# Kernel tuning notes

Measured on AMD Instinct MI355X. Metric: run time of the kernel, lower is better.

## Reference

```python
import jax, jax.numpy as jnp
import numpy as np

N_A, N_B = 100000, 50000
F_IN, C = 32, 64
L, G = 2, 4  # conv layers per gate, gates (i,f,o,c)
E_AA, E_AB, E_BB = 1600000, 800000, 800000


def setup_inputs() -> dict:
    key = jax.random.key(0)
    ks = jax.random.split(key, 15)
    return {
        "x_a": jax.random.normal(ks[0], (N_A, F_IN), jnp.float32),
        "x_b": jax.random.normal(ks[1], (N_B, F_IN), jnp.float32),
        "c_a": jax.random.normal(ks[2], (N_A, C), jnp.float32),
        "c_b": jax.random.normal(ks[3], (N_B, C), jnp.float32),
        "lin_w": jax.random.normal(ks[4], (G, 2, F_IN, C), jnp.float32) * 0.1,
        "lin_b": jax.random.uniform(ks[5], (G, 2, C), jnp.float32),
        "conv_wl": jax.random.normal(ks[6], (G, L, 3, C, C), jnp.float32) * 0.1,
        "conv_wr": jax.random.normal(ks[7], (G, L, 3, C, C), jnp.float32) * 0.1,
        "conv_b": jax.random.uniform(ks[8], (G, L, 3, C), jnp.float32) * 0.1,
        "src_aa": jax.random.randint(ks[9], (E_AA,), 0, N_A),
        "dst_aa": jax.random.randint(ks[10], (E_AA,), 0, N_A),
        "src_ab": jax.random.randint(ks[11], (E_AB,), 0, N_A),
        "dst_ab": jax.random.randint(ks[12], (E_AB,), 0, N_B),
        "src_bb": jax.random.randint(ks[13], (E_BB,), 0, N_B),
        "dst_bb": jax.random.randint(ks[14], (E_BB,), 0, N_B),
    }


def _seg_mean(x_src, src, dst, n_dst):
    # SAGEConv mean aggregation; empty destinations get 0 (PyG semantics)
    s = jax.ops.segment_sum(x_src[src], dst, num_segments=n_dst)
    cnt = jax.ops.segment_sum(jnp.ones((src.shape[0], 1), x_src.dtype), dst, num_segments=n_dst)
    return s / jnp.maximum(cnt, 1.0)


def _gate(g, x_a, x_b, lin_w, lin_b, conv_wl, conv_wr, conv_b, idx):
    src_aa, dst_aa, src_ab, dst_ab, src_bb, dst_bb = idx
    t_a = x_a @ lin_w[g, 0]
    t_b = x_b @ lin_w[g, 1]
    for l in range(L):
        # edge type 0: a->a (dst a)
        agg_aa = _seg_mean(t_a, src_aa, dst_aa, N_A)
        na = agg_aa @ conv_wl[g, l, 0] + t_a @ conv_wr[g, l, 0] + conv_b[g, l, 0]
        # edge types 1: a->b and 2: b->b, HeteroConv sums both into dst b
        agg_ab = _seg_mean(t_a, src_ab, dst_ab, N_B)
        agg_bb = _seg_mean(t_b, src_bb, dst_bb, N_B)
        nb = (agg_ab @ conv_wl[g, l, 1] + t_b @ conv_wr[g, l, 1] + conv_b[g, l, 1]
              + agg_bb @ conv_wl[g, l, 2] + t_b @ conv_wr[g, l, 2] + conv_b[g, l, 2])
        t_a, t_b = na, nb
    return lin_b[g, 0] + t_a, lin_b[g, 1] + t_b


def reference(x_a, x_b, c_a, c_b, lin_w, lin_b, conv_wl, conv_wr, conv_b,
              src_aa, dst_aa, src_ab, dst_ab, src_bb, dst_bb):
    idx = (src_aa, dst_aa, src_ab, dst_ab, src_bb, dst_bb)
    i_a, i_b = map(jax.nn.sigmoid, _gate(0, x_a, x_b, lin_w, lin_b, conv_wl, conv_wr, conv_b, idx))
    f_a, f_b = map(jax.nn.sigmoid, _gate(1, x_a, x_b, lin_w, lin_b, conv_wl, conv_wr, conv_b, idx))
    o_a, o_b = map(jax.nn.sigmoid, _gate(2, x_a, x_b, lin_w, lin_b, conv_wl, conv_wr, conv_b, idx))
    g_a, g_b = map(jnp.tanh, _gate(3, x_a, x_b, lin_w, lin_b, conv_wl, conv_wr, conv_b, idx))
    cn_a = f_a * c_a + i_a * g_a
    cn_b = f_b * c_b + i_b * g_b
    h_a = o_a * jnp.tanh(cn_a)
    h_b = o_b * jnp.tanh(cn_b)
    return (h_a, h_b, cn_a, cn_b)
```

## Files before the change

### kernel.cpp

```cpp
#include <hip/hip_runtime.h>
#include <hip/hip_bf16.h>

#define NA 100000
#define NB 50000
#define EAA 1600000
#define EAB 800000
#define EBB 800000

#define NBKAA 782
#define NBKB  391
#define EPB 2000
#define BKA 800
#define BKB 400
#define DCAP 4096

#define GF2A 782
#define GF2B 391

typedef __hip_bfloat16 bf16;
typedef __attribute__((ext_vector_type(8))) short bf16x8;
typedef __attribute__((ext_vector_type(4))) float f32x4;

__device__ __forceinline__ float u2f(unsigned short u) {
  union { unsigned int i; float f; } x; x.i = ((unsigned int)u) << 16; return x.f;
}
__device__ __forceinline__ unsigned short f2u(float f) {
  __hip_bfloat16 h = __float2bfloat16(f);
  return *reinterpret_cast<unsigned short*>(&h);
}
__device__ __forceinline__ short f2bs(float f) {
  __hip_bfloat16 h = __float2bfloat16(f);
  return *reinterpret_cast<short*>(&h);
}
__device__ __forceinline__ float fast_sigmoid(float z) {
  return 1.f / (1.f + __expf(-z));
}
__device__ __forceinline__ float fast_tanh(float z) {
  z = fminf(fmaxf(z, -15.f), 15.f);
  float t = __expf(2.f * z);
  return (t - 1.f) / (t + 1.f);
}

__global__ __launch_bounds__(256) void kA_bin(
    const int* __restrict__ d1, const int* __restrict__ d2, const int* __restrict__ d3,
    int* __restrict__ binAA, int* __restrict__ binAB, int* __restrict__ binBB) {
  __shared__ int h[1024];
  int blk = blockIdx.x;
  const int* dst; int* out; int e0, nbk;
  if (blk < BKA)            { dst = d1; out = binAA + blk * NBKAA; e0 = blk * EPB; nbk = NBKAA; }
  else if (blk < BKA + BKB) { int k = blk - BKA; dst = d2; out = binAB + k * NBKB; e0 = k * EPB; nbk = NBKB; }
  else                      { int k = blk - BKA - BKB; dst = d3; out = binBB + k * NBKB; e0 = k * EPB; nbk = NBKB; }
  for (int i = threadIdx.x; i < nbk; i += 256) h[i] = 0;
  __syncthreads();
  for (int i = threadIdx.x; i < EPB; i += 256) atomicAdd(&h[dst[e0 + i] >> 7], 1);
  __syncthreads();
  for (int i = threadIdx.x; i < nbk; i += 256) out[i] = h[i];
}

__global__ __launch_bounds__(256) void kB1(
    int* __restrict__ binAA, int* __restrict__ binAB, int* __restrict__ binBB,
    int* __restrict__ totAA, int* __restrict__ totAB, int* __restrict__ totBB) {
  int wave = threadIdx.x >> 6, lane = threadIdx.x & 63;
  int wid = blockIdx.x * 4 + wave;
  int* bin; int* tot; int b, nblk, nbk;
  if (wid < NBKAA)              { bin = binAA; tot = totAA; b = wid; nblk = BKA; nbk = NBKAA; }
  else if (wid < NBKAA + NBKB)  { bin = binAB; tot = totAB; b = wid - NBKAA; nblk = BKB; nbk = NBKB; }
  else                          { bin = binBB; tot = totBB; b = wid - NBKAA - NBKB; nblk = BKB; nbk = NBKB; }
  int C = (nblk + 63) / 64;
  int vals[16]; int s = 0;
  for (int j = 0; j < C; ++j) { int k = lane * C + j; vals[j] = (k < nblk) ? bin[k * nbk + b] : 0; s += vals[j]; }
  int pre = s;
  for (int o = 1; o < 64; o <<= 1) { int x = __shfl_up(pre, o); if (lane >= o) pre += x; }
  int run = pre - s;
  for (int j = 0; j < C; ++j) { int k = lane * C + j; if (k < nblk) { int v = vals[j]; bin[k * nbk + b] = run; run += v; } }
  if (lane == 63) tot[b] = pre;
}

__global__ __launch_bounds__(256) void kB2(
    const int* __restrict__ totAA, const int* __restrict__ totAB, const int* __restrict__ totBB,
    int* __restrict__ bsAA, int* __restrict__ bsAB, int* __restrict__ bsBB) {
  __shared__ int part[256];
  int set = blockIdx.x; const int* tot; int* bs; int nbk;
  if (set == 0)      { tot = totAA; bs = bsAA; nbk = NBKAA; }
  else if (set == 1) { tot = totAB; bs = bsAB; nbk = NBKB; }
  else               { tot = totBB; bs = bsBB; nbk = NBKB; }
  int t = threadIdx.x;
  int v[4]; int s = 0;
  #pragma unroll
  for (int j = 0; j < 4; ++j) { int k = t * 4 + j; v[j] = (k < nbk) ? tot[k] : 0; s += v[j]; }
  part[t] = s;
  __syncthreads();
  for (int o = 1; o < 256; o <<= 1) {
    int x = (t >= o) ? part[t - o] : 0;
    __syncthreads();
    part[t] += x;
    __syncthreads();
  }
  int run = part[t] - s;
  #pragma unroll
  for (int j = 0; j < 4; ++j) { int k = t * 4 + j; if (k < nbk) { bs[k] = run; run += v[j]; } }
  if (t == 255) bs[nbk] = part[255];
}

__global__ __launch_bounds__(256) void kC_scatter(
    const int* __restrict__ s1, const int* __restrict__ d1,
    const int* __restrict__ s2, const int* __restrict__ d2,
    const int* __restrict__ s3, const int* __restrict__ d3,
    const int* __restrict__ binAA, const int* __restrict__ binAB, const int* __restrict__ binBB,
    const int* __restrict__ bsAA, const int* __restrict__ bsAB, const int* __restrict__ bsBB,
    int* __restrict__ pkAA, int* __restrict__ pkAB, int* __restrict__ pkBB) {
  __shared__ int baseL[1024];
  __shared__ int run[1024];
  int blk = blockIdx.x;
  const int* src; const int* dst; const int* bin; const int* bs; int* pk; int e0, nbk, bofs;
  if (blk < BKA)            { src = s1; dst = d1; bin = binAA; bs = bsAA; pk = pkAA; e0 = blk * EPB; nbk = NBKAA; bofs = blk * NBKAA; }
  else if (blk < BKA + BKB) { int k = blk - BKA; src = s2; dst = d2; bin = binAB; bs = bsAB; pk = pkAB; e0 = k * EPB; nbk = NBKB; bofs = k * NBKB; }
  else                      { int k = blk - BKA - BKB; src = s3; dst = d3; bin = binBB; bs = bsBB; pk = pkBB; e0 = k * EPB; nbk = NBKB; bofs = k * NBKB; }
  for (int i = threadIdx.x; i < nbk; i += 256) { baseL[i] = bs[i] + bin[bofs + i]; run[i] = 0; }
  __syncthreads();
  for (int i = threadIdx.x; i < EPB; i += 256) {
    int d = dst[e0 + i];
    int b = d >> 7;
    int off = atomicAdd(&run[b], 1);
    pk[baseL[b] + off] = src[e0 + i] | ((d & 127) << 24);
  }
}

__global__ __launch_bounds__(256) void kD_nodesort(
    const int* __restrict__ pkAA, const int* __restrict__ pkAB, const int* __restrict__ pkBB,
    const int* __restrict__ bsAA, const int* __restrict__ bsAB, const int* __restrict__ bsBB,
    int* __restrict__ colAA, int* __restrict__ colAB, int* __restrict__ colBB,
    int* __restrict__ stAA, int* __restrict__ ctAA,
    int* __restrict__ stAB, int* __restrict__ ctAB,
    int* __restrict__ stBB, int* __restrict__ ctBB) {
  __shared__ int hist[128], nodeOff[129], run[128];
  __shared__ int stage[DCAP];
  int wid = blockIdx.x;
  const int* pk; const int* bs; int* col; int* stn; int* ctn; int b, N;
  if (wid < NBKAA)             { pk = pkAA; bs = bsAA; col = colAA; stn = stAA; ctn = ctAA; b = wid; N = NA; }
  else if (wid < NBKAA + NBKB) { pk = pkAB; bs = bsAB; col = colAB; stn = stAB; ctn = ctAB; b = wid - NBKAA; N = NB; }
  else                         { pk = pkBB; bs = bsBB; col = colBB; stn = stBB; ctn = ctBB; b = wid - NBKAA - NBKB; N = NB; }
  int node0 = b * 128;
  int base = bs[b], cntB = bs[b + 1] - base;
  int t = threadIdx.x;
  if (t < 128) hist[t] = 0;
  __syncthreads();
  for (int i = t; i < cntB; i += 256) atomicAdd(&hist[pk[base + i] >> 24], 1);
  __syncthreads();
  if (t < 64) {
    int v0 = hist[2 * t], v1 = hist[2 * t + 1];
    int s = v0 + v1; int pre = s;
    for (int o = 1; o < 64; o <<= 1) { int x = __shfl_up(pre, o); if (t >= o) pre += x; }
    int ex = pre - s;
    nodeOff[2 * t] = ex; nodeOff[2 * t + 1] = ex + v0;
    if (t == 63) nodeOff[128] = pre;
    run[2 * t] = 0; run[2 * t + 1] = 0;
  }
  __syncthreads();
  if (t < 128) {
    int n = node0 + t;
    if (n < N) { ctn[n] = hist[t]; stn[n] = base + nodeOff[t]; }
  }
  if (cntB <= DCAP) {
    for (int i = t; i < cntB; i += 256) {
      int e = pk[base + i]; int ln = e >> 24;
      int off = atomicAdd(&run[ln], 1);
      stage[nodeOff[ln] + off] = e & 0xFFFFFF;
    }
    __syncthreads();
    for (int i = t; i < cntB; i += 256) col[base + i] = stage[i];
  } else {
    for (int i = t; i < cntB; i += 256) {
      int e = pk[base + i]; int ln = e >> 24;
      int off = atomicAdd(&run[ln], 1);
      col[base + nodeOff[ln] + off] = e & 0xFFFFFF;
    }
  }
}

__global__ __launch_bounds__(256) void k_cast2(const float* __restrict__ xa, const float* __restrict__ xb,
                                               bf16* __restrict__ ya, bf16* __restrict__ yb) {
  int i = blockIdx.x * 256 + threadIdx.x;
  const float* x; bf16* y; int base;
  if (i < 800000)       { x = xa; y = ya; base = i * 4; }
  else if (i < 1200000) { x = xb; y = yb; base = (i - 800000) * 4; }
  else return;
  float4 v = *(const float4*)(x + base);
  ushort4 o; o.x = f2u(v.x); o.y = f2u(v.y); o.z = f2u(v.z); o.w = f2u(v.w);
  *(ushort4*)(y + base) = o;
}

__global__ __launch_bounds__(256) void kW1(
    const float* __restrict__ lin_w, const float* __restrict__ wl, const float* __restrict__ wr,
    float* __restrict__ Mbuf) {
  __shared__ float Ls[32][64];
  __shared__ float Rs[64][64];
  int id = blockIdx.x, term = id >> 2, g = id & 3;
  const float* L = lin_w + ((size_t)g * 2 + (term >= 3 ? 1 : 0)) * 2048;
  const float* R1; const float* R2 = nullptr;
  switch (term) {
    case 0: R1 = wl + ((size_t)(g * 2) * 3 + 0) * 4096; break;
    case 1: R1 = wr + ((size_t)(g * 2) * 3 + 0) * 4096; break;
    case 2: R1 = wl + ((size_t)(g * 2) * 3 + 1) * 4096; break;
    case 3: R1 = wl + ((size_t)(g * 2) * 3 + 2) * 4096; break;
    default: R1 = wr + ((size_t)(g * 2) * 3 + 1) * 4096; R2 = wr + ((size_t)(g * 2) * 3 + 2) * 4096; break;
  }
  for (int i = threadIdx.x; i < 2048; i += 256) Ls[i >> 6][i & 63] = L[i];
  for (int i = threadIdx.x; i < 4096; i += 256) Rs[i >> 6][i & 63] = R2 ? (R1[i] + R2[i]) : R1[i];
  __syncthreads();
  int c = threadIdx.x & 63, rq = threadIdx.x >> 6;
  float acc[8] = {0, 0, 0, 0, 0, 0, 0, 0};
  for (int k = 0; k < 64; ++k) {
    float rv = Rs[k][c];
    #pragma unroll
    for (int i = 0; i < 8; ++i) acc[i] += Ls[rq * 8 + i][k] * rv;
  }
  #pragma unroll
  for (int i = 0; i < 8; ++i)
    Mbuf[(size_t)(term * 4 + g) * 2048 + (rq * 8 + i) * 64 + c] = acc[i];
}

__global__ __launch_bounds__(256) void kW2(
    const float* __restrict__ Mbuf, const float* __restrict__ wl, const float* __restrict__ wr,
    const float* __restrict__ cbv, const float* __restrict__ lin_b,
    bf16* __restrict__ Wfrag, float* __restrict__ Bv) {
  __shared__ float Ps[2][32][65];
  __shared__ float Ws[2][64][64];
  int blk = blockIdx.x;
  if (blk >= 36) {
    int g = blk - 36;
    if (threadIdx.x < 64) {
      int c = threadIdx.x;
      const float* b00 = cbv + (size_t)((g * 2 + 0) * 3 + 0) * 64;
      const float* b10 = cbv + (size_t)((g * 2 + 0) * 3 + 1) * 64;
      const float* b20 = cbv + (size_t)((g * 2 + 0) * 3 + 2) * 64;
      const float* b01 = cbv + (size_t)((g * 2 + 1) * 3 + 0) * 64;
      const float* b11 = cbv + (size_t)((g * 2 + 1) * 3 + 1) * 64;
      const float* b21 = cbv + (size_t)((g * 2 + 1) * 3 + 2) * 64;
      const float* wl01 = wl + (size_t)((g * 2 + 1) * 3 + 0) * 4096;
      const float* wl11 = wl + (size_t)((g * 2 + 1) * 3 + 1) * 4096;
      const float* wl21 = wl + (size_t)((g * 2 + 1) * 3 + 2) * 4096;
      const float* wr01 = wr + (size_t)((g * 2 + 1) * 3 + 0) * 4096;
      const float* wr11 = wr + (size_t)((g * 2 + 1) * 3 + 1) * 4096;
      const float* wr21 = wr + (size_t)((g * 2 + 1) * 3 + 2) * 4096;
      float s_maa = 0.f, s_ca = 0.f, s_mab = 0.f, s_mbb = 0.f, s_cb = 0.f;
      for (int k = 0; k < 64; ++k) {
        float v0 = b00[k], vb = b10[k] + b20[k];
        s_maa += v0 * wl01[k * 64 + c];
        s_ca  += v0 * wr01[k * 64 + c];
        s_mab += v0 * wl11[k * 64 + c];
        s_mbb += vb * wl21[k * 64 + c];
        s_cb  += vb * (wr11[k * 64 + c] + wr21[k * 64 + c]);
      }
      Bv[(g * 5 + 0) * 64 + c] = s_maa;
      Bv[(g * 5 + 1) * 64 + c] = s_ca + b01[c] + lin_b[(g * 2 + 0) * 64 + c];
      Bv[(g * 5 + 2) * 64 + c] = s_mab;
      Bv[(g * 5 + 3) * 64 + c] = s_mbb;
      Bv[(g * 5 + 4) * 64 + c] = s_cb + b11[c] + b21[c] + lin_b[(g * 2 + 1) * 64 + c];
    }
    return;
  }
  int mat = blk, g, m;
  if (blk < 12) { g = blk / 3; m = blk % 3; }
  else          { g = (blk - 12) / 6; m = (blk - 12) % 6 + 3; }
  const float* wl01 = wl + (size_t)((g * 2 + 1) * 3 + 0) * 4096;
  const float* wl11 = wl + (size_t)((g * 2 + 1) * 3 + 1) * 4096;
  const float* wl21 = wl + (size_t)((g * 2 + 1) * 3 + 2) * 4096;
  const float* wr01 = wr + (size_t)((g * 2 + 1) * 3 + 0) * 4096;
  const float* wr11 = wr + (size_t)((g * 2 + 1) * 3 + 1) * 4096;
  const float* wr21 = wr + (size_t)((g * 2 + 1) * 3 + 2) * 4096;
  int   p1t, p2t = -1;
  const float *w1a = nullptr, *w1b = nullptr, *w2a = nullptr, *w2b = nullptr;
  switch (m) {
    case 0: p1t = 0; w1a = wl01; break;
    case 1: p1t = 1; w1a = wl01; p2t = 0; w2a = wr01; break;
    case 2: p1t = 1; w1a = wr01; break;
    case 3: p1t = 0; w1a = wl11; break;
    case 4: p1t = 1; w1a = wl11; p2t = 2; w2a = wr11; w2b = wr21; break;
    case 5: p1t = 2; w1a = wl21; break;
    case 6: p1t = 3; w1a = wl21; break;
    case 7: p1t = 3; w1a = wr11; w1b = wr21; p2t = 4; w2a = wl21; break;
    default: p1t = 4; w1a = wr11; w1b = wr21; break;
  }
  int nprod = (p2t >= 0) ? 2 : 1;
  for (int i = threadIdx.x; i < 2048; i += 256) Ps[0][i >> 6][i & 63] = Mbuf[(size_t)(p1t * 4 + g) * 2048 + i];
  for (int i = threadIdx.x; i < 4096; i += 256) Ws[0][i >> 6][i & 63] = w1b ? (w1a[i] + w1b[i]) : w1a[i];
  if (nprod == 2) {
    for (int i = threadIdx.x; i < 2048; i += 256) Ps[1][i >> 6][i & 63] = Mbuf[(size_t)(p2t * 4 + g) * 2048 + i];
    for (int i = threadIdx.x; i < 4096; i += 256) Ws[1][i >> 6][i & 63] = w2b ? (w2a[i] + w2b[i]) : w2a[i];
  }
  __syncthreads();
  int nt = threadIdx.x >> 6, lane = threadIdx.x & 63;
  int c = nt * 16 + (lane & 15), kb = (lane >> 4) * 8;
  float acc[8] = {0, 0, 0, 0, 0, 0, 0, 0};
  for (int k = 0; k < 64; ++k) {
    float w1v = Ws[0][k][c];
    #pragma unroll
    for (int j = 0; j < 8; ++j) acc[j] += Ps[0][kb + j][k] * w1v;
  }
  if (nprod == 2) {
    for (int k = 0; k < 64; ++k) {
      float w2v = Ws[1][k][c];
      #pragma unroll
      for (int j = 0; j < 8; ++j) acc[j] += Ps[1][kb + j][k] * w2v;
    }
  }
  bf16x8 v;
  #pragma unroll
  for (int j = 0; j < 8; ++j) v[j] = f2bs(acc[j]);
  *(bf16x8*)(Wfrag + ((size_t)(mat * 4 + nt) * 64 + lane) * 8) = v;
}

__device__ __forceinline__ void acc8(float* s, uint4 v) {
  s[0] += u2f((unsigned short)(v.x & 0xFFFF)); s[1] += u2f((unsigned short)(v.x >> 16));
  s[2] += u2f((unsigned short)(v.y & 0xFFFF)); s[3] += u2f((unsigned short)(v.y >> 16));
  s[4] += u2f((unsigned short)(v.z & 0xFFFF)); s[5] += u2f((unsigned short)(v.z >> 16));
  s[6] += u2f((unsigned short)(v.w & 0xFFFF)); s[7] += u2f((unsigned short)(v.w >> 16));
}
__device__ __forceinline__ void red16(float* s) {
  #pragma unroll
  for (int j = 0; j < 8; ++j) {
    s[j] += __shfl_xor(s[j], 4);
    s[j] += __shfl_xor(s[j], 8);
    s[j] += __shfl_xor(s[j], 16);
    s[j] += __shfl_xor(s[j], 32);
  }
}
__device__ __forceinline__ uint4 pack8(const float* s, float inv) {
  uint4 o;
  o.x = (unsigned)f2u(s[0] * inv) | ((unsigned)f2u(s[1] * inv) << 16);
  o.y = (unsigned)f2u(s[2] * inv) | ((unsigned)f2u(s[3] * inv) << 16);
  o.z = (unsigned)f2u(s[4] * inv) | ((unsigned)f2u(s[5] * inv) << 16);
  o.w = (unsigned)f2u(s[6] * inv) | ((unsigned)f2u(s[7] * inv) << 16);
  return o;
}

__global__ __launch_bounds__(256) void k_aggP1(
    const bf16* __restrict__ xa, const bf16* __restrict__ xb,
    bf16* __restrict__ P, bf16* __restrict__ Q, bf16* __restrict__ R,
    const int* __restrict__ st_aa, const int* __restrict__ ct_aa, const int* __restrict__ col_aa,
    const int* __restrict__ st_ab, const int* __restrict__ ct_ab, const int* __restrict__ col_ab,
    const int* __restrict__ st_bb, const int* __restrict__ ct_bb, const int* __restrict__ col_bb) {
  int b = blockIdx.x;
  const bf16* src; bf16* dst; const int* start; const int* cnt; const int* col; int n0;
  if (b < 25000)      { src = xa; dst = P; start = st_aa; cnt = ct_aa; col = col_aa; n0 = b * 4; }
  else if (b < 37500) { src = xa; dst = Q; start = st_ab; cnt = ct_ab; col = col_ab; n0 = (b - 25000) * 4; }
  else                { src = xb; dst = R; start = st_bb; cnt = ct_bb; col = col_bb; n0 = (b - 37500) * 4; }
  int wave = threadIdx.x >> 6, lane = threadIdx.x & 63;
  int n = n0 + wave;
  int e16 = lane >> 2, c4 = lane & 3;
  int st = start[n];
  int deg = cnt[n];
  float s[8] = {0, 0, 0, 0, 0, 0, 0, 0};
  for (int e = e16; e < deg; e += 16) {
    int i = col[st + e];
    uint4 v = *(const uint4*)(src + (size_t)i * 32 + c4 * 8);
    acc8(s, v);
  }
  red16(s);
  if (e16 == 0) {
    float inv = 1.f / (float)(deg > 1 ? deg : 1);
    *(uint4*)(dst + (size_t)n * 32 + c4 * 8) = pack8(s, inv);
  }
}

__global__ __launch_bounds__(256) void k_aggP2(
    const bf16* __restrict__ P, const bf16* __restrict__ Q, const bf16* __restrict__ R,
    bf16* __restrict__ P2, bf16* __restrict__ Q2, bf16* __restrict__ S, bf16* __restrict__ T,
    const int* __restrict__ st_aa, const int* __restrict__ ct_aa, const int* __restrict__ col_aa,
    const int* __restrict__ st_ab, const int* __restrict__ ct_ab, const int* __restrict__ col_ab,
    const int* __restrict__ st_bb, const int* __restrict__ ct_bb, const int* __restrict__ col_bb) {
  int b = blockIdx.x;
  int wave = threadIdx.x >> 6, lane = threadIdx.x & 63;
  int e16 = lane >> 2, c4 = lane & 3;
  if (b < 37500) {
    const bf16* src; bf16* dst; const int* start; const int* cnt; const int* col; int n0;
    if (b < 25000) { src = P; dst = P2; start = st_aa; cnt = ct_aa; col = col_aa; n0 = b * 4; }
    else           { src = P; dst = Q2; start = st_ab; cnt = ct_ab; col = col_ab; n0 = (b - 25000) * 4; }
    int n = n0 + wave;
    int st = start[n];
    int deg = cnt[n];
    float s[8] = {0, 0, 0, 0, 0, 0, 0, 0};
    for (int e = e16; e < deg; e += 16) {
      int i = col[st + e];
      uint4 v = *(const uint4*)(src + (size_t)i * 32 + c4 * 8);
      acc8(s, v);
    }
    red16(s);
    if (e16 == 0) {
      float inv = 1.f / (float)(deg > 1 ? deg : 1);
      *(uint4*)(dst + (size_t)n * 32 + c4 * 8) = pack8(s, inv);
    }
  } else {
    int n = (b - 37500) * 4 + wave;
    int st = st_bb[n];
    int deg = ct_bb[n];
    float sq[8] = {0, 0, 0, 0, 0, 0, 0, 0};
    float sr[8] = {0, 0, 0, 0, 0, 0, 0, 0};
    for (int e = e16; e < deg; e += 16) {
      int i = col_bb[st + e];
      uint4 vq = *(const uint4*)(Q + (size_t)i * 32 + c4 * 8);
      uint4 vr = *(const uint4*)(R + (size_t)i * 32 + c4 * 8);
      acc8(sq, vq);
      acc8(sr, vr);
    }
    red16(sq);
    red16(sr);
    if (e16 == 0) {
      float inv = 1.f / (float)(deg > 1 ? deg : 1);
      *(uint4*)(S + (size_t)n * 32 + c4 * 8) = pack8(sq, inv);
      *(uint4*)(T + (size_t)n * 32 + c4 * 8) = pack8(sr, inv);
    }
  }
}

__global__ __launch_bounds__(256) void k_fin(
    const bf16* __restrict__ xa, const bf16* __restrict__ P, const bf16* __restrict__ P2,
    const bf16* __restrict__ xb, const bf16* __restrict__ Q, const bf16* __restrict__ R,
    const bf16* __restrict__ Q2, const bf16* __restrict__ S, const bf16* __restrict__ T,
    const bf16* __restrict__ Wfrag, const float* __restrict__ Bv,
    const int* __restrict__ cnt_aa, const int* __restrict__ cnt_ab, const int* __restrict__ cnt_bb,
    const float* __restrict__ c_a, const float* __restrict__ c_b,
    float* __restrict__ out) {
  int blk = blockIdx.x;
  int wave = threadIdx.x >> 6, lane = threadIdx.x & 63;
  int l15 = lane & 15, l4 = lane >> 4;
  const size_t TOTA = (size_t)NA * 64, TOTB = (size_t)NB * 64;
  #define FRAG(mat, nt) (*(const bf16x8*)(Wfrag + ((size_t)((mat) * 4 + (nt)) * 64 + lane) * 8))
  const bf16x8 z8 = {0, 0, 0, 0, 0, 0, 0, 0};

  if (blk < GF2A) {
    int row0 = (blk * 4 + wave) * 32;
    bf16x8 a[3][2];
    float m[2][4];
    #pragma unroll
    for (int s = 0; s < 2; ++s) {
      int r = row0 + s * 16 + l15;
      bool ok = r < NA;
      a[0][s] = ok ? *(const bf16x8*)(P2 + (size_t)r * 32 + l4 * 8) : z8;
      a[1][s] = ok ? *(const bf16x8*)(P  + (size_t)r * 32 + l4 * 8) : z8;
      a[2][s] = ok ? *(const bf16x8*)(xa + (size_t)r * 32 + l4 * 8) : z8;
      #pragma unroll
      for (int q = 0; q < 4; ++q) {
        int rr = row0 + s * 16 + l4 * 4 + q;
        m[s][q] = (rr < NA && cnt_aa[rr] > 0) ? 1.f : 0.f;
      }
    }
    float* h = out;
    float* cn = out + TOTA + TOTB;
    #pragma unroll
    for (int nt = 0; nt < 4; ++nt) {
      int col = nt * 16 + l15;
      bf16x8 fr[12];
      #pragma unroll
      for (int gq = 0; gq < 12; ++gq) fr[gq] = FRAG(gq, nt);
      float bm[4], bc[4];
      #pragma unroll
      for (int g = 0; g < 4; ++g) { bm[g] = Bv[(g * 5 + 0) * 64 + col]; bc[g] = Bv[(g * 5 + 1) * 64 + col]; }
      #pragma unroll
      for (int s = 0; s < 2; ++s) {
        float cpre[4];
        #pragma unroll
        for (int q = 0; q < 4; ++q) {
          int rr = row0 + s * 16 + l4 * 4 + q;
          cpre[q] = (rr < NA) ? c_a[(size_t)rr * 64 + col] : 0.f;
        }
        f32x4 z[4];
        #pragma unroll
        for (int g = 0; g < 4; ++g) {
          f32x4 acc = {0.f, 0.f, 0.f, 0.f};
          acc = __builtin_amdgcn_mfma_f32_16x16x32_bf16(a[0][s], fr[g * 3 + 0], acc, 0, 0, 0);
          acc = __builtin_amdgcn_mfma_f32_16x16x32_bf16(a[1][s], fr[g * 3 + 1], acc, 0, 0, 0);
          acc = __builtin_amdgcn_mfma_f32_16x16x32_bf16(a[2][s], fr[g * 3 + 2], acc, 0, 0, 0);
          z[g] = acc;
        }
        #pragma unroll
        for (int q = 0; q < 4; ++q) {
          int rr = row0 + s * 16 + l4 * 4 + q;
          if (rr >= NA) continue;
          float zi = z[0][q] + m[s][q] * bm[0] + bc[0];
          float zf = z[1][q] + m[s][q] * bm[1] + bc[1];
          float zo = z[2][q] + m[s][q] * bm[2] + bc[2];
          float zg = z[3][q] + m[s][q] * bm[3] + bc[3];
          float ig = fast_sigmoid(zi);
          float fg = fast_sigmoid(zf);
          float og = fast_sigmoid(zo);
          float gg = fast_tanh(zg);
          size_t idx = (size_t)rr * 64 + col;
          float cv = fg * cpre[q] + ig * gg;
          h[idx] = og * fast_tanh(cv);
          cn[idx] = cv;
        }
      }
    }
  } else {
    int bb = blk - GF2A;
    int row0 = (bb * 4 + wave) * 32;
    bf16x8 a[6][2];
    float mab[2][4], mbb[2][4];
    #pragma unroll
    for (int s = 0; s < 2; ++s) {
      int r = row0 + s * 16 + l15;
      bool ok = r < NB;
      a[0][s] = ok ? *(const bf16x8*)(Q2 + (size_t)r * 32 + l4 * 8) : z8;
      a[1][s] = ok ? *(const bf16x8*)(Q  + (size_t)r * 32 + l4 * 8) : z8;
      a[2][s] = ok ? *(const bf16x8*)(S  + (size_t)r * 32 + l4 * 8) : z8;
      a[3][s] = ok ? *(const bf16x8*)(T  + (size_t)r * 32 + l4 * 8) : z8;
      a[4][s] = ok ? *(const bf16x8*)(R  + (size_t)r * 32 + l4 * 8) : z8;
      a[5][s] = ok ? *(const bf16x8*)(xb + (size_t)r * 32 + l4 * 8) : z8;
      #pragma unroll
      for (int q = 0; q < 4; ++q) {
        int rr = row0 + s * 16 + l4 * 4 + q;
        bool okr = rr < NB;
        mab[s][q] = (okr && cnt_ab[rr] > 0) ? 1.f : 0.f;
        mbb[s][q] = (okr && cnt_bb[rr] > 0) ? 1.f : 0.f;
      }
    }
    float* h = out + TOTA;
    float* cn = out + 2 * TOTA + TOTB;
    #pragma unroll
    for (int nt = 0; nt < 4; ++nt) {
      int col = nt * 16 + l15;
      float bm1[4], bm2[4], bc[4];
      #pragma unroll
      for (int g = 0; g < 4; ++g) {
        bm1[g] = Bv[(g * 5 + 2) * 64 + col];
        bm2[g] = Bv[(g * 5 + 3) * 64 + col];
        bc[g]  = Bv[(g * 5 + 4) * 64 + col];
      }
      float cpre[2][4];
      #pragma unroll
      for (int s = 0; s < 2; ++s)
        #pragma unroll
        for (int q = 0; q < 4; ++q) {
          int rr = row0 + s * 16 + l4 * 4 + q;
          cpre[s][q] = (rr < NB) ? c_b[(size_t)rr * 64 + col] : 0.f;
        }
      f32x4 z[2][4];
      #pragma unroll
      for (int s = 0; s < 2; ++s)
        #pragma unroll
        for (int g = 0; g < 4; ++g) z[s][g] = (f32x4){0.f, 0.f, 0.f, 0.f};
      #pragma unroll
      for (int g = 0; g < 4; ++g) {
        bf16x8 fr[6];
        #pragma unroll
        for (int t = 0; t < 6; ++t) fr[t] = FRAG(12 + g * 6 + t, nt);
        #pragma unroll
        for (int s = 0; s < 2; ++s) {
          #pragma unroll
          for (int t = 0; t < 6; ++t)
            z[s][g] = __builtin_amdgcn_mfma_f32_16x16x32_bf16(a[t][s], fr[t], z[s][g], 0, 0, 0);
        }
      }
      #pragma unroll
      for (int s = 0; s < 2; ++s) {
        #pragma unroll
        for (int q = 0; q < 4; ++q) {
          int rr = row0 + s * 16 + l4 * 4 + q;
          if (rr >= NB) continue;
          float zi = z[s][0][q] + mab[s][q] * bm1[0] + mbb[s][q] * bm2[0] + bc[0];
          float zf = z[s][1][q] + mab[s][q] * bm1[1] + mbb[s][q] * bm2[1] + bc[1];
          float zo = z[s][2][q] + mab[s][q] * bm1[2] + mbb[s][q] * bm2[2] + bc[2];
          float zg = z[s][3][q] + mab[s][q] * bm1[3] + mbb[s][q] * bm2[3] + bc[3];
          float ig = fast_sigmoid(zi);
          float fg = fast_sigmoid(zf);
          float og = fast_sigmoid(zo);
          float gg = fast_tanh(zg);
          size_t idx = (size_t)rr * 64 + col;
          float cv = fg * cpre[s][q] + ig * gg;
          h[idx] = og * fast_tanh(cv);
          cn[idx] = cv;
        }
      }
    }
  }
  #undef FRAG
}

extern "C" void kernel_launch(void* const* d_in, const int* in_sizes, int n_in,
                              void* d_out, int out_size, void* d_ws, size_t ws_size,
                              hipStream_t stream) {
  (void)in_sizes; (void)n_in; (void)out_size; (void)ws_size;
  const float* x_a    = (const float*)d_in[0];
  const float* x_b    = (const float*)d_in[1];
  const float* c_a    = (const float*)d_in[2];
  const float* c_b    = (const float*)d_in[3];
  const float* lin_w  = (const float*)d_in[4];
  const float* lin_b  = (const float*)d_in[5];
  const float* conv_wl = (const float*)d_in[6];
  const float* conv_wr = (const float*)d_in[7];
  const float* conv_cb = (const float*)d_in[8];
  const int* src_aa = (const int*)d_in[9];
  const int* dst_aa = (const int*)d_in[10];
  const int* src_ab = (const int*)d_in[11];
  const int* dst_ab = (const int*)d_in[12];
  const int* src_bb = (const int*)d_in[13];
  const int* dst_bb = (const int*)d_in[14];

  char* ws = (char*)d_ws;
  size_t off = 0;
  auto alloc = [&](size_t bytes) -> char* {
    off = (off + 255) & ~(size_t)255;
    char* p = ws + off;
    off += bytes;
    return p;
  };
  bf16* xab = (bf16*)alloc((size_t)NA * 32 * 2);
  bf16* xbb = (bf16*)alloc((size_t)NB * 32 * 2);
  bf16* P   = (bf16*)alloc((size_t)NA * 32 * 2);
  bf16* P2  = (bf16*)alloc((size_t)NA * 32 * 2);
  bf16* Q   = (bf16*)alloc((size_t)NB * 32 * 2);
  bf16* R   = (bf16*)alloc((size_t)NB * 32 * 2);
  bf16* Q2  = (bf16*)alloc((size_t)NB * 32 * 2);
  bf16* S   = (bf16*)alloc((size_t)NB * 32 * 2);
  bf16* T   = (bf16*)alloc((size_t)NB * 32 * 2);
  float* Mbuf = (float*)alloc((size_t)20 * 2048 * 4);
  bf16* Wfrag = (bf16*)alloc((size_t)36 * 4 * 64 * 8 * 2);
  float* Bv = (float*)alloc((size_t)4 * 5 * 64 * 4);
  int* col_aa  = (int*)alloc((size_t)EAA * 4);
  int* col_ab  = (int*)alloc((size_t)EAB * 4);
  int* col_bb  = (int*)alloc((size_t)EBB * 4);
  int* pk_aa   = (int*)alloc((size_t)EAA * 4);
  int* pk_ab   = (int*)alloc((size_t)EAB * 4);
  int* pk_bb   = (int*)alloc((size_t)EBB * 4);
  int* start_aa = (int*)alloc((size_t)NA * 4);
  int* start_ab = (int*)alloc((size_t)NB * 4);
  int* start_bb = (int*)alloc((size_t)NB * 4);
  int* cnt_aa  = (int*)alloc((size_t)NA * 4);
  int* cnt_ab  = (int*)alloc((size_t)NB * 4);
  int* cnt_bb  = (int*)alloc((size_t)NB * 4);
  int* binAA   = (int*)alloc((size_t)BKA * NBKAA * 4);
  int* binAB   = (int*)alloc((size_t)BKB * NBKB * 4);
  int* binBB   = (int*)alloc((size_t)BKB * NBKB * 4);
  int* totAA   = (int*)alloc((size_t)NBKAA * 4);
  int* totAB   = (int*)alloc((size_t)NBKB * 4);
  int* totBB   = (int*)alloc((size_t)NBKB * 4);
  int* bsAA    = (int*)alloc((size_t)(NBKAA + 1) * 4);
  int* bsAB    = (int*)alloc((size_t)(NBKB + 1) * 4);
  int* bsBB    = (int*)alloc((size_t)(NBKB + 1) * 4);

  kW1<<<20, 256, 0, stream>>>(lin_w, conv_wl, conv_wr, Mbuf);
  kW2<<<40, 256, 0, stream>>>(Mbuf, conv_wl, conv_wr, conv_cb, lin_b, Wfrag, Bv);
  k_cast2<<<4688, 256, 0, stream>>>(x_a, x_b, xab, xbb);

  kA_bin<<<BKA + 2 * BKB, 256, 0, stream>>>(dst_aa, dst_ab, dst_bb, binAA, binAB, binBB);
  kB1<<<(NBKAA + 2 * NBKB) / 4, 256, 0, stream>>>(binAA, binAB, binBB, totAA, totAB, totBB);
  kB2<<<3, 256, 0, stream>>>(totAA, totAB, totBB, bsAA, bsAB, bsBB);
  kC_scatter<<<BKA + 2 * BKB, 256, 0, stream>>>(src_aa, dst_aa, src_ab, dst_ab, src_bb, dst_bb,
                                                binAA, binAB, binBB, bsAA, bsAB, bsBB,
                                                pk_aa, pk_ab, pk_bb);
  kD_nodesort<<<NBKAA + 2 * NBKB, 256, 0, stream>>>(pk_aa, pk_ab, pk_bb, bsAA, bsAB, bsBB,
                                                    col_aa, col_ab, col_bb,
                                                    start_aa, cnt_aa, start_ab, cnt_ab,
                                                    start_bb, cnt_bb);

  k_aggP1<<<50000, 256, 0, stream>>>(xab, xbb, P, Q, R,
                                     start_aa, cnt_aa, col_aa,
                                     start_ab, cnt_ab, col_ab,
                                     start_bb, cnt_bb, col_bb);
  k_aggP2<<<50000, 256, 0, stream>>>(P, Q, R, P2, Q2, S, T,
                                     start_aa, cnt_aa, col_aa,
                                     start_ab, cnt_ab, col_ab,
                                     start_bb, cnt_bb, col_bb);

  k_fin<<<GF2A + GF2B, 256, 0, stream>>>(xab, P, P2, xbb, Q, R, Q2, S, T,
                                         Wfrag, Bv, cnt_aa, cnt_ab, cnt_bb,
                                         c_a, c_b, (float*)d_out);
}
```

Measured before the change: 334.3 us.

## Use fewer, larger binning blocks and remap aggregation lanes to 4 edges x 16 channel pairs

The bin and scatter kernels now process 8000 edges per block with a quarter as many blocks, which shrinks the per-block histogram matrix and the column scan in kB1. The aggregation kernels change the wave layout from 16 edges by 4 lanes of 8 channels (16-byte loads) to 4 edges by 16 lanes of 2 channels (4-byte loads), with fewer registers and a shorter shuffle reduction. The aim is to cut reduction and prefix-sum overhead and to improve per-row coalescing of the gathers. The cost is smaller per-lane loads, fewer edges in flight per wave, and less parallelism in the binning stage.

```diff
diff --git a/kernel.cpp b/kernel.cpp
--- a/kernel.cpp
+++ b/kernel.cpp
@@ -9,9 +9,8 @@
 
 #define NBKAA 782
 #define NBKB  391
-#define EPB 2000
-#define BKA 800
-#define BKB 400
+#define BKA 200
+#define BKB 100
 #define DCAP 4096
 
 #define GF2A 782
@@ -47,12 +46,12 @@
   __shared__ int h[1024];
   int blk = blockIdx.x;
   const int* dst; int* out; int e0, nbk;
-  if (blk < BKA)            { dst = d1; out = binAA + blk * NBKAA; e0 = blk * EPB; nbk = NBKAA; }
-  else if (blk < BKA + BKB) { int k = blk - BKA; dst = d2; out = binAB + k * NBKB; e0 = k * EPB; nbk = NBKB; }
-  else                      { int k = blk - BKA - BKB; dst = d3; out = binBB + k * NBKB; e0 = k * EPB; nbk = NBKB; }
+  if (blk < BKA)            { dst = d1; out = binAA + blk * NBKAA; e0 = blk * 8000; nbk = NBKAA; }
+  else if (blk < BKA + BKB) { int k = blk - BKA; dst = d2; out = binAB + k * NBKB; e0 = k * 8000; nbk = NBKB; }
+  else                      { int k = blk - BKA - BKB; dst = d3; out = binBB + k * NBKB; e0 = k * 8000; nbk = NBKB; }
   for (int i = threadIdx.x; i < nbk; i += 256) h[i] = 0;
   __syncthreads();
-  for (int i = threadIdx.x; i < EPB; i += 256) atomicAdd(&h[dst[e0 + i] >> 7], 1);
+  for (int i = threadIdx.x; i < 8000; i += 256) atomicAdd(&h[dst[e0 + i] >> 7], 1);
   __syncthreads();
   for (int i = threadIdx.x; i < nbk; i += 256) out[i] = h[i];
 }
@@ -67,7 +66,7 @@
   else if (wid < NBKAA + NBKB)  { bin = binAB; tot = totAB; b = wid - NBKAA; nblk = BKB; nbk = NBKB; }
   else                          { bin = binBB; tot = totBB; b = wid - NBKAA - NBKB; nblk = BKB; nbk = NBKB; }
   int C = (nblk + 63) / 64;
-  int vals[16]; int s = 0;
+  int vals[4]; int s = 0;
   for (int j = 0; j < C; ++j) { int k = lane * C + j; vals[j] = (k < nblk) ? bin[k * nbk + b] : 0; s += vals[j]; }
   int pre = s;
   for (int o = 1; o < 64; o <<= 1) { int x = __shfl_up(pre, o); if (lane >= o) pre += x; }
@@ -113,12 +112,12 @@
   __shared__ int run[1024];
   int blk = blockIdx.x;
   const int* src; const int* dst; const int* bin; const int* bs; int* pk; int e0, nbk, bofs;
-  if (blk < BKA)            { src = s1; dst = d1; bin = binAA; bs = bsAA; pk = pkAA; e0 = blk * EPB; nbk = NBKAA; bofs = blk * NBKAA; }
-  else if (blk < BKA + BKB) { int k = blk - BKA; src = s2; dst = d2; bin = binAB; bs = bsAB; pk = pkAB; e0 = k * EPB; nbk = NBKB; bofs = k * NBKB; }
-  else                      { int k = blk - BKA - BKB; src = s3; dst = d3; bin = binBB; bs = bsBB; pk = pkBB; e0 = k * EPB; nbk = NBKB; bofs = k * NBKB; }
+  if (blk < BKA)            { src = s1; dst = d1; bin = binAA; bs = bsAA; pk = pkAA; e0 = blk * 8000; nbk = NBKAA; bofs = blk * NBKAA; }
+  else if (blk < BKA + BKB) { int k = blk - BKA; src = s2; dst = d2; bin = binAB; bs = bsAB; pk = pkAB; e0 = k * 8000; nbk = NBKB; bofs = k * NBKB; }
+  else                      { int k = blk - BKA - BKB; src = s3; dst = d3; bin = binBB; bs = bsBB; pk = pkBB; e0 = k * 8000; nbk = NBKB; bofs = k * NBKB; }
   for (int i = threadIdx.x; i < nbk; i += 256) { baseL[i] = bs[i] + bin[bofs + i]; run[i] = 0; }
   __syncthreads();
-  for (int i = threadIdx.x; i < EPB; i += 256) {
+  for (int i = threadIdx.x; i < 8000; i += 256) {
     int d = dst[e0 + i];
     int b = d >> 7;
     int off = atomicAdd(&run[b], 1);
@@ -311,30 +310,6 @@
   *(bf16x8*)(Wfrag + ((size_t)(mat * 4 + nt) * 64 + lane) * 8) = v;
 }
 
-__device__ __forceinline__ void acc8(float* s, uint4 v) {
-  s[0] += u2f((unsigned short)(v.x & 0xFFFF)); s[1] += u2f((unsigned short)(v.x >> 16));
-  s[2] += u2f((unsigned short)(v.y & 0xFFFF)); s[3] += u2f((unsigned short)(v.y >> 16));
-  s[4] += u2f((unsigned short)(v.z & 0xFFFF)); s[5] += u2f((unsigned short)(v.z >> 16));
-  s[6] += u2f((unsigned short)(v.w & 0xFFFF)); s[7] += u2f((unsigned short)(v.w >> 16));
-}
-__device__ __forceinline__ void red16(float* s) {
-  #pragma unroll
-  for (int j = 0; j < 8; ++j) {
-    s[j] += __shfl_xor(s[j], 4);
-    s[j] += __shfl_xor(s[j], 8);
-    s[j] += __shfl_xor(s[j], 16);
-    s[j] += __shfl_xor(s[j], 32);
-  }
-}
-__device__ __forceinline__ uint4 pack8(const float* s, float inv) {
-  uint4 o;
-  o.x = (unsigned)f2u(s[0] * inv) | ((unsigned)f2u(s[1] * inv) << 16);
-  o.y = (unsigned)f2u(s[2] * inv) | ((unsigned)f2u(s[3] * inv) << 16);
-  o.z = (unsigned)f2u(s[4] * inv) | ((unsigned)f2u(s[5] * inv) << 16);
-  o.w = (unsigned)f2u(s[6] * inv) | ((unsigned)f2u(s[7] * inv) << 16);
-  return o;
-}
-
 __global__ __launch_bounds__(256) void k_aggP1(
     const bf16* __restrict__ xa, const bf16* __restrict__ xb,
     bf16* __restrict__ P, bf16* __restrict__ Q, bf16* __restrict__ R,
@@ -348,19 +323,23 @@
   else                { src = xb; dst = R; start = st_bb; cnt = ct_bb; col = col_bb; n0 = (b - 37500) * 4; }
   int wave = threadIdx.x >> 6, lane = threadIdx.x & 63;
   int n = n0 + wave;
-  int e16 = lane >> 2, c4 = lane & 3;
+  int e4 = lane >> 4, c16 = lane & 15;
   int st = start[n];
   int deg = cnt[n];
-  float s[8] = {0, 0, 0, 0, 0, 0, 0, 0};
-  for (int e = e16; e < deg; e += 16) {
+  float s0 = 0.f, s1 = 0.f;
+  #pragma unroll 4
+  for (int e = e4; e < deg; e += 4) {
     int i = col[st + e];
-    uint4 v = *(const uint4*)(src + (size_t)i * 32 + c4 * 8);
-    acc8(s, v);
-  }
-  red16(s);
-  if (e16 == 0) {
+    ushort2 v = *(const ushort2*)(src + (size_t)i * 32 + c16 * 2);
+    s0 += u2f(v.x);
+    s1 += u2f(v.y);
+  }
+  s0 += __shfl_xor(s0, 16); s1 += __shfl_xor(s1, 16);
+  s0 += __shfl_xor(s0, 32); s1 += __shfl_xor(s1, 32);
+  if (e4 == 0) {
     float inv = 1.f / (float)(deg > 1 ? deg : 1);
-    *(uint4*)(dst + (size_t)n * 32 + c4 * 8) = pack8(s, inv);
+    ushort2 o; o.x = f2u(s0 * inv); o.y = f2u(s1 * inv);
+    *(ushort2*)(dst + (size_t)n * 32 + c16 * 2) = o;
   }
 }
 
@@ -372,7 +351,7 @@
     const int* __restrict__ st_bb, const int* __restrict__ ct_bb, const int* __restrict__ col_bb) {
   int b = blockIdx.x;
   int wave = threadIdx.x >> 6, lane = threadIdx.x & 63;
-  int e16 = lane >> 2, c4 = lane & 3;
+  int e4 = lane >> 4, c16 = lane & 15;
   if (b < 37500) {
     const bf16* src; bf16* dst; const int* start; const int* cnt; const int* col; int n0;
     if (b < 25000) { src = P; dst = P2; start = st_aa; cnt = ct_aa; col = col_aa; n0 = b * 4; }
@@ -380,36 +359,44 @@
     int n = n0 + wave;
     int st = start[n];
     int deg = cnt[n];
-    float s[8] = {0, 0, 0, 0, 0, 0, 0, 0};
-    for (int e = e16; e < deg; e += 16) {
+    float s0 = 0.f, s1 = 0.f;
+    #pragma unroll 4
+    for (int e = e4; e < deg; e += 4) {
       int i = col[st + e];
-      uint4 v = *(const uint4*)(src + (size_t)i * 32 + c4 * 8);
-      acc8(s, v);
-    }
-    red16(s);
-    if (e16 == 0) {
+      ushort2 v = *(const ushort2*)(src + (size_t)i * 32 + c16 * 2);
+      s0 += u2f(v.x);
+      s1 += u2f(v.y);
+    }
+    s0 += __shfl_xor(s0, 16); s1 += __shfl_xor(s1, 16);
+    s0 += __shfl_xor(s0, 32); s1 += __shfl_xor(s1, 32);
+    if (e4 == 0) {
       float inv = 1.f / (float)(deg > 1 ? deg : 1);
-      *(uint4*)(dst + (size_t)n * 32 + c4 * 8) = pack8(s, inv);
+      ushort2 o; o.x = f2u(s0 * inv); o.y = f2u(s1 * inv);
+      *(ushort2*)(dst + (size_t)n * 32 + c16 * 2) = o;
     }
   } else {
     int n = (b - 37500) * 4 + wave;
     int st = st_bb[n];
     int deg = ct_bb[n];
-    float sq[8] = {0, 0, 0, 0, 0, 0, 0, 0};
-    float sr[8] = {0, 0, 0, 0, 0, 0, 0, 0};
-    for (int e = e16; e < deg; e += 16) {
+    float q0 = 0.f, q1 = 0.f, r0 = 0.f, r1 = 0.f;
+    #pragma unroll 2
+    for (int e = e4; e < deg; e += 4) {
       int i = col_bb[st + e];
-      uint4 vq = *(const uint4*)(Q + (size_t)i * 32 + c4 * 8);
-      uint4 vr = *(const uint4*)(R + (size_t)i * 32 + c4 * 8);
-      acc8(sq, vq);
-      acc8(sr, vr);
-    }
-    red16(sq);
-    red16(sr);
-    if (e16 == 0) {
+      ushort2 vq = *(const ushort2*)(Q + (size_t)i * 32 + c16 * 2);
+      ushort2 vr = *(const ushort2*)(R + (size_t)i * 32 + c16 * 2);
+      q0 += u2f(vq.x); q1 += u2f(vq.y);
+      r0 += u2f(vr.x); r1 += u2f(vr.y);
+    }
+    q0 += __shfl_xor(q0, 16); q1 += __shfl_xor(q1, 16);
+    r0 += __shfl_xor(r0, 16); r1 += __shfl_xor(r1, 16);
+    q0 += __shfl_xor(q0, 32); q1 += __shfl_xor(q1, 32);
+    r0 += __shfl_xor(r0, 32); r1 += __shfl_xor(r1, 32);
+    if (e4 == 0) {
       float inv = 1.f / (float)(deg > 1 ? deg : 1);
-      *(uint4*)(S + (size_t)n * 32 + c4 * 8) = pack8(sq, inv);
-      *(uint4*)(T + (size_t)n * 32 + c4 * 8) = pack8(sr, inv);
+      ushort2 o1v; o1v.x = f2u(q0 * inv); o1v.y = f2u(q1 * inv);
+      *(ushort2*)(S + (size_t)n * 32 + c16 * 2) = o1v;
+      ushort2 o2v; o2v.x = f2u(r0 * inv); o2v.y = f2u(r1 * inv);
+      *(ushort2*)(T + (size_t)n * 32 + c16 * 2) = o2v;
     }
   }
 }
```

Measured after the change: 317.5 us. 1.05x faster.
